# Optimization experiments

Hardware: AMD Instinct MI355X
Metric: run time of the kernel (lower is better)

The kernel has to match this reference:

```python
import jax, jax.numpy as jnp
import numpy as np

B, G = 32, 8          # batch, num_genres
N, T = 64, 64         # notes_size, timestep_size (input)
D, O = 32, 32         # notes_out, timestep_out (output)


def setup_inputs() -> dict:
    key = jax.random.key(0)
    k1, k2, k3, k4, k5 = jax.random.split(key, 5)
    x = jax.random.normal(k1, (B, N, T), dtype=jnp.float32)
    y = jax.random.uniform(k2, (B, G), dtype=jnp.float32)
    weight = jax.random.normal(k3, (G, D, O, N, T), dtype=jnp.float32) * 0.02
    bias = jax.random.normal(k4, (D * O,), dtype=jnp.float32) * 0.02
    mask = jax.random.randint(k5, (O, T), 0, 2).astype(jnp.float32)
    return {"x": x, "y": y, "weight": weight, "bias": bias, "mask": mask}


def reference(x, y, weight, bias, mask):
    # Fused form of:
    #   mw  = einsum('gdont,ot->gdont', weight, mask)
    #   mw2 = einsum('gdont,bg->bdont', mw, y)      # huge intermediate avoided
    #   out = einsum('bnt,bdont->bdo', x, mw2) + bias
    mw = weight * mask[None, None, :, None, :]          # (g,d,o,n,t)
    xw = jnp.einsum('bnt,gdont->bgdo', x, mw)           # contract n,t first
    out = jnp.einsum('bg,bgdo->bdo', y, xw)             # (b,d,o)
    return out + bias.reshape(D, O)[None, :, :]
```

## Files before the change

kernel.cpp:

```cpp
#include <hip/hip_runtime.h>
#include <hip/hip_bf16.h>

typedef __bf16 bf16x8 __attribute__((ext_vector_type(8)));
typedef float f32x4 __attribute__((ext_vector_type(4)));

#define G 8
#define B 32
#define D 32
#define O 32
#define K 4096
#define T 64
#define KSPLIT 2
#define KCHUNK (K / KSPLIT)
#define BK 256
#define NSTEP (KCHUNK / BK)
#define MROWS 16

#define XB_ELEMS (B * K)

__global__ __launch_bounds__(256) void prep_and_init(const float* __restrict__ x,
                                                     const float* __restrict__ bias,
                                                     __bf16* __restrict__ xb,
                                                     float* __restrict__ out) {
    int tid = blockIdx.x * 256 + threadIdx.x;
    if (tid < 16384) {
        int b = (tid >> 2) & 31;
        int k = (tid >> 7) * 32 + (tid & 3) * 8;
        const float4 x0 = *(const float4*)(x + b * K + k);
        const float4 x1 = *(const float4*)(x + b * K + k + 4);
        bf16x8 r;
        r[0] = (__bf16)x0.x; r[1] = (__bf16)x0.y; r[2] = (__bf16)x0.z; r[3] = (__bf16)x0.w;
        r[4] = (__bf16)x1.x; r[5] = (__bf16)x1.y; r[6] = (__bf16)x1.z; r[7] = (__bf16)x1.w;
        *(bf16x8*)(xb + (size_t)tid * 8) = r;
    } else {
        int t2 = tid - 16384;
        out[t2] = bias[t2 & 1023];
    }
}

__global__ __launch_bounds__(128) void gemm_main(const float* __restrict__ W,
                                                 const __bf16* __restrict__ xb,
                                                 const float* __restrict__ mask,
                                                 const float* __restrict__ y,
                                                 float* __restrict__ out) {
    __shared__ float ldsW[2][MROWS * BK];
    const int d = blockIdx.x, g = blockIdx.y;
    const int oh = blockIdx.z & 1, ks = blockIdx.z >> 1;
    const int wid  = threadIdx.x >> 6;
    const int lane = threadIdx.x & 63;
    const int bh = wid;
    const int l15 = lane & 15, g16 = lane >> 4;

    const int lds_ro = l15 * 1024 + ((g16 * 32) ^ ((l15 & 7) * 16));

    const float* mrow = mask + (oh * 16 + l15) * T + g16 * 8;
    const float4 me0 = *(const float4*)(mrow);
    const float4 me1 = *(const float4*)(mrow + 4);
    const float4 mo0 = *(const float4*)(mrow + 32);
    const float4 mo1 = *(const float4*)(mrow + 36);

    const __bf16* xbl = xb + (size_t)(ks * (KCHUNK / 32)) * 1024
                           + (bh * 16 + l15) * 32 + g16 * 8;

    const size_t wrow0 = ((size_t)(g * D + d) * O + oh * 16 + 8 * wid) * K
                         + (size_t)ks * KCHUNK;

    f32x4 acc = {0.f, 0.f, 0.f, 0.f};

#define STAGE(buf, step)                                                          \
    {                                                                             \
        _Pragma("unroll")                                                         \
        for (int i = 0; i < 8; ++i) {                                             \
            const int row = 8 * wid + i;                                          \
            const char* src = (const char*)(W + wrow0 + (size_t)i * K             \
                                            + (size_t)(step) * BK)                \
                              + ((lane * 16) ^ (i * 16));                         \
            __builtin_amdgcn_global_load_lds(                                     \
                (const __attribute__((address_space(1))) void*)src,               \
                (__attribute__((address_space(3))) void*)((char*)&ldsW[buf][0]    \
                                                          + row * 1024),          \
                16, 0, 0);                                                        \
        }                                                                         \
    }

    STAGE(0, 0);
    __syncthreads();

    int cur = 0;
    for (int step = 0; step < NSTEP; ++step) {
        if (step + 1 < NSTEP) STAGE(cur ^ 1, step + 1);

        const char* lb = (const char*)&ldsW[cur][0];
        const __bf16* xs = xbl + (size_t)(step * 8) * 1024;
        #pragma unroll
        for (int s = 0; s < 8; ++s) {
            const int a0 = lds_ro + s * 128;
            const f32x4 alo = *(const f32x4*)(lb + a0);
            const f32x4 ahi = *(const f32x4*)(lb + (a0 ^ 16));
            const float4 ms0 = (s & 1) ? mo0 : me0;
            const float4 ms1 = (s & 1) ? mo1 : me1;
            bf16x8 af;
            af[0] = (__bf16)(alo[0] * ms0.x); af[1] = (__bf16)(alo[1] * ms0.y);
            af[2] = (__bf16)(alo[2] * ms0.z); af[3] = (__bf16)(alo[3] * ms0.w);
            af[4] = (__bf16)(ahi[0] * ms1.x); af[5] = (__bf16)(ahi[1] * ms1.y);
            af[6] = (__bf16)(ahi[2] * ms1.z); af[7] = (__bf16)(ahi[3] * ms1.w);
            const bf16x8 bfr = *(const bf16x8*)(xs + (size_t)s * 1024);
            acc = __builtin_amdgcn_mfma_f32_16x16x32_bf16(af, bfr, acc, 0, 0, 0);
        }
        __syncthreads();
        cur ^= 1;
    }
#undef STAGE

    const int bg = bh * 16 + l15;
    const float yv = y[bg * G + g];
    float* op = out + bg * (D * O) + d * O + oh * 16;
    #pragma unroll
    for (int i = 0; i < 4; ++i)
        unsafeAtomicAdd(op + g16 * 4 + i, yv * acc[i]);
}

extern "C" void kernel_launch(void* const* d_in, const int* in_sizes, int n_in,
                              void* d_out, int out_size, void* d_ws, size_t ws_size,
                              hipStream_t stream) {
    const float* x    = (const float*)d_in[0];
    const float* y    = (const float*)d_in[1];
    const float* w    = (const float*)d_in[2];
    const float* bias = (const float*)d_in[3];
    const float* mask = (const float*)d_in[4];
    float* out = (float*)d_out;

    __bf16* xbp = (__bf16*)d_ws;

    prep_and_init<<<192, 256, 0, stream>>>(x, bias, xbp, out);
    gemm_main<<<dim3(D, G, 4), 128, 0, stream>>>(w, xbp, mask, y, out);
}
```

Baseline: 35.16 us.

## Prefetch x fragments into registers and use explicit vmcnt waits for pipelining

Per K-step, all eight bf16 x fragments are loaded into registers before issuing the next W stage's global_load_lds. A manual s_waitcnt vmcnt(8) plus raw s_barrier replaces __syncthreads, so the next stage's prefetch can stay in flight while the current buffer is consumed. The loop is fully unrolled and sched_barriers pin instruction order. This relies on exact in-order counting of vector memory ops and adds register pressure.

```diff
diff --git a/kernel.cpp b/kernel.cpp
--- a/kernel.cpp
+++ b/kernel.cpp
@@ -83,15 +83,35 @@
         }                                                                         \
     }
 
+    bf16x8 xr[8];
+#define XLOAD(step)                                                               \
+    {                                                                             \
+        _Pragma("unroll")                                                         \
+        for (int s = 0; s < 8; ++s)                                               \
+            xr[s] = *(const bf16x8*)(xbl + (size_t)(step) * 8192                  \
+                                         + (size_t)s * 1024);                     \
+    }
+
     STAGE(0, 0);
-    __syncthreads();
 
-    int cur = 0;
+    #pragma unroll
     for (int step = 0; step < NSTEP; ++step) {
-        if (step + 1 < NSTEP) STAGE(cur ^ 1, step + 1);
+        const int cur = step & 1;
+
+        XLOAD(step);
+        __builtin_amdgcn_sched_barrier(0);
+        if (step + 1 < NSTEP) {
+            STAGE(cur ^ 1, step + 1);
+            __builtin_amdgcn_sched_barrier(0);
+            asm volatile("s_waitcnt vmcnt(8)" ::: "memory");
+        } else {
+            __builtin_amdgcn_sched_barrier(0);
+            asm volatile("s_waitcnt vmcnt(0)" ::: "memory");
+        }
+        __builtin_amdgcn_s_barrier();
+        __builtin_amdgcn_sched_barrier(0);
 
         const char* lb = (const char*)&ldsW[cur][0];
-        const __bf16* xs = xbl + (size_t)(step * 8) * 1024;
         #pragma unroll
         for (int s = 0; s < 8; ++s) {
             const int a0 = lds_ro + s * 128;
@@ -104,13 +124,15 @@
             af[2] = (__bf16)(alo[2] * ms0.z); af[3] = (__bf16)(alo[3] * ms0.w);
             af[4] = (__bf16)(ahi[0] * ms1.x); af[5] = (__bf16)(ahi[1] * ms1.y);
             af[6] = (__bf16)(ahi[2] * ms1.z); af[7] = (__bf16)(ahi[3] * ms1.w);
-            const bf16x8 bfr = *(const bf16x8*)(xs + (size_t)s * 1024);
-            acc = __builtin_amdgcn_mfma_f32_16x16x32_bf16(af, bfr, acc, 0, 0, 0);
+            acc = __builtin_amdgcn_mfma_f32_16x16x32_bf16(af, xr[s], acc, 0, 0, 0);
         }
-        __syncthreads();
-        cur ^= 1;
+
+        __builtin_amdgcn_sched_barrier(0);
+        asm volatile("s_waitcnt lgkmcnt(0)" ::: "memory");
+        __builtin_amdgcn_s_barrier();
     }
 #undef STAGE
+#undef XLOAD
 
     const int bg = bh * 16 + l15;
     const float yv = y[bg * G + g];
```

New measurement: 36.01 us. +2.4%, slower.

## Stage weights through registers, single LDS buffer, split K across four waves

Applied to the files above, without the earlier changes.

Replaces the double-buffered direct global-to-LDS loads with register-staged loads that are written to a single LDS buffer, with the next tile prefetched into registers during compute. Doubles the block to four waves and splits each 256-wide K step between wave pairs, then reduces the two partial accumulators through LDS before the atomic adds. The goal is more memory-level parallelism and occupancy for a weight-streaming, bandwidth-bound GEMM, at the cost of extra syncthreads per step, more register use and an extra LDS reduction.

```diff
diff --git a/kernel.cpp b/kernel.cpp
--- a/kernel.cpp
+++ b/kernel.cpp
@@ -38,17 +38,17 @@
     }
 }
 
-__global__ __launch_bounds__(128) void gemm_main(const float* __restrict__ W,
-                                                 const __bf16* __restrict__ xb,
-                                                 const float* __restrict__ mask,
-                                                 const float* __restrict__ y,
-                                                 float* __restrict__ out) {
-    __shared__ float ldsW[2][MROWS * BK];
+__global__ __launch_bounds__(256, 4) void gemm_main(const float* __restrict__ W,
+                                                    const __bf16* __restrict__ xb,
+                                                    const float* __restrict__ mask,
+                                                    const float* __restrict__ y,
+                                                    float* __restrict__ out) {
+    __shared__ float ldsW[MROWS * BK];
     const int d = blockIdx.x, g = blockIdx.y;
     const int oh = blockIdx.z & 1, ks = blockIdx.z >> 1;
     const int wid  = threadIdx.x >> 6;
     const int lane = threadIdx.x & 63;
-    const int bh = wid;
+    const int bh = wid & 1, kh = wid >> 1;
     const int l15 = lane & 15, g16 = lane >> 4;
 
     const int lds_ro = l15 * 1024 + ((g16 * 32) ^ ((l15 & 7) * 16));
@@ -62,62 +62,94 @@
     const __bf16* xbl = xb + (size_t)(ks * (KCHUNK / 32)) * 1024
                            + (bh * 16 + l15) * 32 + g16 * 8;
 
-    const size_t wrow0 = ((size_t)(g * D + d) * O + oh * 16 + 8 * wid) * K
-                         + (size_t)ks * KCHUNK;
+    const size_t wrow0 = ((size_t)(g * D + d) * O + oh * 16) * K + (size_t)ks * KCHUNK;
 
     f32x4 acc = {0.f, 0.f, 0.f, 0.f};
 
-#define STAGE(buf, step)                                                          \
+#define REGLOAD(wreg, step)                                                       \
     {                                                                             \
         _Pragma("unroll")                                                         \
-        for (int i = 0; i < 8; ++i) {                                             \
-            const int row = 8 * wid + i;                                          \
-            const char* src = (const char*)(W + wrow0 + (size_t)i * K             \
-                                            + (size_t)(step) * BK)                \
-                              + ((lane * 16) ^ (i * 16));                         \
-            __builtin_amdgcn_global_load_lds(                                     \
-                (const __attribute__((address_space(1))) void*)src,               \
-                (__attribute__((address_space(3))) void*)((char*)&ldsW[buf][0]    \
-                                                          + row * 1024),          \
-                16, 0, 0);                                                        \
+        for (int j = 0; j < 4; ++j)                                               \
+            wreg[j] = *(const f32x4*)(W + wrow0 + (size_t)(wid * 4 + j) * K       \
+                                      + (step) * BK + lane * 4);                  \
+    }
+#define XLOAD(xreg, step)                                                         \
+    {                                                                             \
+        _Pragma("unroll")                                                         \
+        for (int s2 = 0; s2 < 4; ++s2)                                            \
+            xreg[s2] = *(const bf16x8*)(xbl + ((size_t)(step) * 8 + kh * 4 + s2)  \
+                                              * 1024);                            \
+    }
+#define DSWRITE(wreg)                                                             \
+    {                                                                             \
+        _Pragma("unroll")                                                         \
+        for (int j = 0; j < 4; ++j) {                                             \
+            const int row = wid * 4 + j;                                          \
+            *(f32x4*)((char*)ldsW + row * 1024                                    \
+                      + ((lane * 16) ^ ((row & 7) * 16))) = wreg[j];              \
+        }                                                                         \
+    }
+#define COMPUTE(xreg)                                                             \
+    {                                                                             \
+        _Pragma("unroll")                                                         \
+        for (int s2 = 0; s2 < 4; ++s2) {                                          \
+            const int ktl = kh * 4 + s2;                                          \
+            const int a0 = lds_ro + ktl * 128;                                    \
+            const f32x4 alo = *(const f32x4*)((char*)ldsW + a0);                  \
+            const f32x4 ahi = *(const f32x4*)((char*)ldsW + (a0 ^ 16));           \
+            const float4 ms0 = (ktl & 1) ? mo0 : me0;                             \
+            const float4 ms1 = (ktl & 1) ? mo1 : me1;                             \
+            bf16x8 af;                                                            \
+            af[0] = (__bf16)(alo[0] * ms0.x); af[1] = (__bf16)(alo[1] * ms0.y);   \
+            af[2] = (__bf16)(alo[2] * ms0.z); af[3] = (__bf16)(alo[3] * ms0.w);   \
+            af[4] = (__bf16)(ahi[0] * ms1.x); af[5] = (__bf16)(ahi[1] * ms1.y);   \
+            af[6] = (__bf16)(ahi[2] * ms1.z); af[7] = (__bf16)(ahi[3] * ms1.w);   \
+            acc = __builtin_amdgcn_mfma_f32_16x16x32_bf16(af, xreg[s2], acc,      \
+                                                          0, 0, 0);               \
         }                                                                         \
     }
 
-    STAGE(0, 0);
-    __syncthreads();
+    f32x4 wrA[4], wrB[4];
+    bf16x8 xA[4], xB[4];
 
-    int cur = 0;
-    for (int step = 0; step < NSTEP; ++step) {
-        if (step + 1 < NSTEP) STAGE(cur ^ 1, step + 1);
+    REGLOAD(wrA, 0);
+    XLOAD(xA, 0);
 
-        const char* lb = (const char*)&ldsW[cur][0];
-        const __bf16* xs = xbl + (size_t)(step * 8) * 1024;
-        #pragma unroll
-        for (int s = 0; s < 8; ++s) {
-            const int a0 = lds_ro + s * 128;
-            const f32x4 alo = *(const f32x4*)(lb + a0);
-            const f32x4 ahi = *(const f32x4*)(lb + (a0 ^ 16));
-            const float4 ms0 = (s & 1) ? mo0 : me0;
-            const float4 ms1 = (s & 1) ? mo1 : me1;
-            bf16x8 af;
-            af[0] = (__bf16)(alo[0] * ms0.x); af[1] = (__bf16)(alo[1] * ms0.y);
-            af[2] = (__bf16)(alo[2] * ms0.z); af[3] = (__bf16)(alo[3] * ms0.w);
-            af[4] = (__bf16)(ahi[0] * ms1.x); af[5] = (__bf16)(ahi[1] * ms1.y);
-            af[6] = (__bf16)(ahi[2] * ms1.z); af[7] = (__bf16)(ahi[3] * ms1.w);
-            const bf16x8 bfr = *(const bf16x8*)(xs + (size_t)s * 1024);
-            acc = __builtin_amdgcn_mfma_f32_16x16x32_bf16(af, bfr, acc, 0, 0, 0);
+    for (int sp = 0; sp < NSTEP; sp += 2) {
+        DSWRITE(wrA);
+        REGLOAD(wrB, sp + 1);
+        XLOAD(xB, sp + 1);
+        __syncthreads();
+        COMPUTE(xA);
+        __syncthreads();
+
+        DSWRITE(wrB);
+        if (sp + 2 < NSTEP) {
+            REGLOAD(wrA, sp + 2);
+            XLOAD(xA, sp + 2);
         }
         __syncthreads();
-        cur ^= 1;
+        COMPUTE(xB);
+        __syncthreads();
     }
-#undef STAGE
+#undef REGLOAD
+#undef XLOAD
+#undef DSWRITE
+#undef COMPUTE
 
-    const int bg = bh * 16 + l15;
-    const float yv = y[bg * G + g];
-    float* op = out + bg * (D * O) + d * O + oh * 16;
-    #pragma unroll
-    for (int i = 0; i < 4; ++i)
-        unsafeAtomicAdd(op + g16 * 4 + i, yv * acc[i]);
+    if (kh == 1)
+        *(f32x4*)((char*)ldsW + (bh * 64 + lane) * 16) = acc;
+    __syncthreads();
+    if (kh == 0) {
+        const f32x4 other = *(const f32x4*)((char*)ldsW + (bh * 64 + lane) * 16);
+        acc += other;
+        const int bg = bh * 16 + l15;
+        const float yv = y[bg * G + g];
+        float* op = out + bg * (D * O) + d * O + oh * 16 + g16 * 4;
+        #pragma unroll
+        for (int i = 0; i < 4; ++i)
+            unsafeAtomicAdd(op + i, yv * acc[i]);
+    }
 }
 
 extern "C" void kernel_launch(void* const* d_in, const int* in_sizes, int n_in,
@@ -133,5 +165,5 @@
     __bf16* xbp = (__bf16*)d_ws;
 
     prep_and_init<<<192, 256, 0, stream>>>(x, bias, xbp, out);
-    gemm_main<<<dim3(D, G, 4), 128, 0, stream>>>(w, xbp, mask, y, out);
+    gemm_main<<<dim3(D, G, 4), 256, 0, stream>>>(w, xbp, mask, y, out);
 }
```

After: 43.68 us. 1.24x slower.

## Process both o-halves per block and split K four ways instead

Applied to the files above, without the earlier changes.

Each block now covers all 32 o rows, holding two accumulators that share the same x fragment per MFMA step. The K dimension is split into four chunks instead of two, so the grid size stays the same. The aim is to reuse each x B-fragment load across two MFMAs and double the work per LDS stage. In exchange, the LDS footprint doubles to 64KB, which may reduce occupancy, and there are twice as many per-thread atomics into the output with more K-split contention per address.

```diff
diff --git a/kernel.cpp b/kernel.cpp
--- a/kernel.cpp
+++ b/kernel.cpp
@@ -10,11 +10,11 @@
 #define O 32
 #define K 4096
 #define T 64
-#define KSPLIT 2
+#define KSPLIT 4
 #define KCHUNK (K / KSPLIT)
 #define BK 256
 #define NSTEP (KCHUNK / BK)
-#define MROWS 16
+#define MROWS 32
 
 #define XB_ELEMS (B * K)
 
@@ -44,37 +44,43 @@
                                                  const float* __restrict__ y,
                                                  float* __restrict__ out) {
     __shared__ float ldsW[2][MROWS * BK];
-    const int d = blockIdx.x, g = blockIdx.y;
-    const int oh = blockIdx.z & 1, ks = blockIdx.z >> 1;
+    const int d = blockIdx.x, g = blockIdx.y, ks = blockIdx.z;
     const int wid  = threadIdx.x >> 6;
     const int lane = threadIdx.x & 63;
     const int bh = wid;
     const int l15 = lane & 15, g16 = lane >> 4;
 
-    const int lds_ro = l15 * 1024 + ((g16 * 32) ^ ((l15 & 7) * 16));
+    const int lds_lo = l15 * 1024 + ((g16 * 32) ^ ((l15 & 7) * 16));
+    const int lds_hi = lds_lo + 16 * 1024;
 
-    const float* mrow = mask + (oh * 16 + l15) * T + g16 * 8;
-    const float4 me0 = *(const float4*)(mrow);
-    const float4 me1 = *(const float4*)(mrow + 4);
-    const float4 mo0 = *(const float4*)(mrow + 32);
-    const float4 mo1 = *(const float4*)(mrow + 36);
+    const float* mlo = mask + l15 * T + g16 * 8;
+    const float4 le0 = *(const float4*)(mlo);
+    const float4 le1 = *(const float4*)(mlo + 4);
+    const float4 lo0 = *(const float4*)(mlo + 32);
+    const float4 lo1 = *(const float4*)(mlo + 36);
+    const float* mhi = mask + (16 + l15) * T + g16 * 8;
+    const float4 he0 = *(const float4*)(mhi);
+    const float4 he1 = *(const float4*)(mhi + 4);
+    const float4 ho0 = *(const float4*)(mhi + 32);
+    const float4 ho1 = *(const float4*)(mhi + 36);
 
     const __bf16* xbl = xb + (size_t)(ks * (KCHUNK / 32)) * 1024
                            + (bh * 16 + l15) * 32 + g16 * 8;
 
-    const size_t wrow0 = ((size_t)(g * D + d) * O + oh * 16 + 8 * wid) * K
+    const size_t wrow0 = ((size_t)(g * D + d) * O + 16 * wid) * K
                          + (size_t)ks * KCHUNK;
 
-    f32x4 acc = {0.f, 0.f, 0.f, 0.f};
+    f32x4 accL = {0.f, 0.f, 0.f, 0.f};
+    f32x4 accH = {0.f, 0.f, 0.f, 0.f};
 
 #define STAGE(buf, step)                                                          \
     {                                                                             \
         _Pragma("unroll")                                                         \
-        for (int i = 0; i < 8; ++i) {                                             \
-            const int row = 8 * wid + i;                                          \
+        for (int i = 0; i < 16; ++i) {                                            \
+            const int row = 16 * wid + i;                                         \
             const char* src = (const char*)(W + wrow0 + (size_t)i * K             \
                                             + (size_t)(step) * BK)                \
-                              + ((lane * 16) ^ (i * 16));                         \
+                              + ((lane * 16) ^ ((i & 7) * 16));                   \
             __builtin_amdgcn_global_load_lds(                                     \
                 (const __attribute__((address_space(1))) void*)src,               \
                 (__attribute__((address_space(3))) void*)((char*)&ldsW[buf][0]    \
@@ -94,18 +100,34 @@
         const __bf16* xs = xbl + (size_t)(step * 8) * 1024;
         #pragma unroll
         for (int s = 0; s < 8; ++s) {
-            const int a0 = lds_ro + s * 128;
-            const f32x4 alo = *(const f32x4*)(lb + a0);
-            const f32x4 ahi = *(const f32x4*)(lb + (a0 ^ 16));
-            const float4 ms0 = (s & 1) ? mo0 : me0;
-            const float4 ms1 = (s & 1) ? mo1 : me1;
-            bf16x8 af;
-            af[0] = (__bf16)(alo[0] * ms0.x); af[1] = (__bf16)(alo[1] * ms0.y);
-            af[2] = (__bf16)(alo[2] * ms0.z); af[3] = (__bf16)(alo[3] * ms0.w);
-            af[4] = (__bf16)(ahi[0] * ms1.x); af[5] = (__bf16)(ahi[1] * ms1.y);
-            af[6] = (__bf16)(ahi[2] * ms1.z); af[7] = (__bf16)(ahi[3] * ms1.w);
             const bf16x8 bfr = *(const bf16x8*)(xs + (size_t)s * 1024);
-            acc = __builtin_amdgcn_mfma_f32_16x16x32_bf16(af, bfr, acc, 0, 0, 0);
+
+            {
+                const int a0 = lds_lo + s * 128;
+                const f32x4 alo = *(const f32x4*)(lb + a0);
+                const f32x4 ahi = *(const f32x4*)(lb + (a0 ^ 16));
+                const float4 ms0 = (s & 1) ? lo0 : le0;
+                const float4 ms1 = (s & 1) ? lo1 : le1;
+                bf16x8 af;
+                af[0] = (__bf16)(alo[0] * ms0.x); af[1] = (__bf16)(alo[1] * ms0.y);
+                af[2] = (__bf16)(alo[2] * ms0.z); af[3] = (__bf16)(alo[3] * ms0.w);
+                af[4] = (__bf16)(ahi[0] * ms1.x); af[5] = (__bf16)(ahi[1] * ms1.y);
+                af[6] = (__bf16)(ahi[2] * ms1.z); af[7] = (__bf16)(ahi[3] * ms1.w);
+                accL = __builtin_amdgcn_mfma_f32_16x16x32_bf16(af, bfr, accL, 0, 0, 0);
+            }
+            {
+                const int a0 = lds_hi + s * 128;
+                const f32x4 alo = *(const f32x4*)(lb + a0);
+                const f32x4 ahi = *(const f32x4*)(lb + (a0 ^ 16));
+                const float4 ms0 = (s & 1) ? ho0 : he0;
+                const float4 ms1 = (s & 1) ? ho1 : he1;
+                bf16x8 af;
+                af[0] = (__bf16)(alo[0] * ms0.x); af[1] = (__bf16)(alo[1] * ms0.y);
+                af[2] = (__bf16)(alo[2] * ms0.z); af[3] = (__bf16)(alo[3] * ms0.w);
+                af[4] = (__bf16)(ahi[0] * ms1.x); af[5] = (__bf16)(ahi[1] * ms1.y);
+                af[6] = (__bf16)(ahi[2] * ms1.z); af[7] = (__bf16)(ahi[3] * ms1.w);
+                accH = __builtin_amdgcn_mfma_f32_16x16x32_bf16(af, bfr, accH, 0, 0, 0);
+            }
         }
         __syncthreads();
         cur ^= 1;
@@ -114,10 +136,12 @@
 
     const int bg = bh * 16 + l15;
     const float yv = y[bg * G + g];
-    float* op = out + bg * (D * O) + d * O + oh * 16;
+    float* op = out + bg * (D * O) + d * O;
     #pragma unroll
-    for (int i = 0; i < 4; ++i)
-        unsafeAtomicAdd(op + g16 * 4 + i, yv * acc[i]);
+    for (int i = 0; i < 4; ++i) {
+        unsafeAtomicAdd(op + g16 * 4 + i,      yv * accL[i]);
+        unsafeAtomicAdd(op + 16 + g16 * 4 + i, yv * accH[i]);
+    }
 }
 
 extern "C" void kernel_launch(void* const* d_in, const int* in_sizes, int n_in,
@@ -133,5 +157,5 @@
     __bf16* xbp = (__bf16*)d_ws;
 
     prep_and_init<<<192, 256, 0, stream>>>(x, bias, xbp, out);
-    gemm_main<<<dim3(D, G, 4), 128, 0, stream>>>(w, xbp, mask, y, out);
+    gemm_main<<<dim3(D, G, KSPLIT), 128, 0, stream>>>(w, xbp, mask, y, out);
 }
```

New measurement: 49.10 us. 1.4x slower.
